# Performance work log

Measured on AMD Instinct MI355X. Metric: run time of the kernel, lower is better.

Reference implementation:

```python
import jax, jax.numpy as jnp
import numpy as np

N_NODES = 100000


def gcn_conv(x, edge_index, W, b):
    # PyG GCNConv: add self-loops, symmetric normalization D^-1/2 (A+I) D^-1/2, then linear.
    n = x.shape[0]
    loop = jnp.arange(n, dtype=edge_index.dtype)
    src = jnp.concatenate([edge_index[0], loop])
    dst = jnp.concatenate([edge_index[1], loop])
    deg = jax.ops.segment_sum(jnp.ones_like(dst, dtype=x.dtype), dst, num_segments=n)
    dinv = jnp.where(deg > 0, jax.lax.rsqrt(deg), 0.0)
    norm = dinv[src] * dinv[dst]                      # [E+N]
    h = x @ W                                          # [N, out]
    msg = h[src] * norm[:, None]                       # gather + scale
    out = jax.ops.segment_sum(msg, dst, num_segments=n)  # scatter-add
    return out + b


def forward_one(x, edge_index, W1, b1, W2, b2, fc_w, fc_b):
    x = jax.nn.relu(gcn_conv(x, edge_index, W1, b1))
    x = jax.nn.relu(gcn_conv(x, edge_index, W2, b2))
    x = jnp.mean(x, axis=0)                            # [hidden]
    return x @ fc_w.T + fc_b


def setup_inputs() -> dict:
    key = jax.random.key(0)
    ks = jax.random.split(key, 10)
    d_in, d_h = 64, 64
    E = 1600000
    s = 1.0 / np.sqrt(d_in)
    return {
        "x1": jax.random.normal(ks[0], (N_NODES, d_in), jnp.float32),
        "x2": jax.random.normal(ks[1], (N_NODES, d_in), jnp.float32),
        "edge_index1": jax.random.randint(ks[2], (2, E), 0, N_NODES, jnp.int32),
        "edge_index2": jax.random.randint(ks[3], (2, E), 0, N_NODES, jnp.int32),
        "W1": jax.random.normal(ks[4], (d_in, d_h), jnp.float32) * s,
        "b1": jnp.zeros((d_h,), jnp.float32),
        "W2": jax.random.normal(ks[5], (d_h, d_h), jnp.float32) * s,
        "b2": jnp.zeros((d_h,), jnp.float32),
        "fc_w": jax.random.normal(ks[6], (d_h, d_h), jnp.float32) * s,
        "fc_b": jnp.zeros((d_h,), jnp.float32),
    }


def reference(x1, x2, edge_index1, edge_index2, W1, b1, W2, b2, fc_w, fc_b):
    out1 = forward_one(x1, edge_index1, W1, b1, W2, b2, fc_w, fc_b)
    out2 = forward_one(x2, edge_index2, W1, b1, W2, b2, fc_w, fc_b)
    return (out1, out2)
```

## Files before the change

kernel.cpp:

```cpp
#include <hip/hip_runtime.h>


#define TPB    256
#define CHUNK  128
#define SHIFT  7
#define KMAX   1024
#define CAP    2560
#define EPB    8192
#define CPAD   16

typedef __attribute__((ext_vector_type(8))) short short8;
typedef __attribute__((ext_vector_type(4))) float f32x4;
typedef __attribute__((ext_vector_type(2))) float float2v;

struct Ctx {
    const float* X; const int* esrc; const int* edst;
    unsigned int* temp; unsigned char* Hs2; unsigned char* Hs;
    unsigned int* csr; int* row_ptr; int* degA; float* dinv; int* cursorG;
    float* P; float* P2; float* outp;
};

__device__ __forceinline__ unsigned short f2bf(float x) {
    union { float f; unsigned int i; } c; c.f = x;
    unsigned int r = c.i + 0x7FFFu + ((c.i >> 16) & 1u);
    return (unsigned short)(r >> 16);
}
__device__ __forceinline__ unsigned char f2fp8(float x) {
    int p = __builtin_amdgcn_cvt_pk_fp8_f32(x, x, 0, false);
    return (unsigned char)(p & 0xFF);
}
__device__ __forceinline__ float2v up8lo(unsigned int w) {
    return __builtin_amdgcn_cvt_pk_f32_fp8(w, false);
}
__device__ __forceinline__ float2v up8hi(unsigned int w) {
    return __builtin_amdgcn_cvt_pk_f32_fp8(w, true);
}

__global__ void k_prepW2(const float* __restrict__ W1, const float* __restrict__ W2,
                         unsigned short* __restrict__ Wt1, unsigned short* __restrict__ Wt2) {
    const float* W = blockIdx.x ? W2 : W1;
    unsigned short* Wt = blockIdx.x ? Wt2 : Wt1;
    for (int i = threadIdx.x; i < 64 * 64; i += 256) {
        int n = i >> 6, k = i & 63;
        Wt[i] = f2bf(W[k * 64 + n]);
    }
}

__global__ void k_zeroCur(Ctx c0, Ctx c1, int nb0, int K, int N) {
    int b = blockIdx.x; Ctx c = c0;
    if (b >= nb0) { c = c1; b -= nb0; }
    int i = b * blockDim.x + threadIdx.x;
    if (i < K) c.cursorG[i * CPAD] = 0;
    if (b == 0 && threadIdx.x < 64) c.Hs[(size_t)N * 64 + threadIdx.x] = 0;
}

__global__ __launch_bounds__(1024) void k_binA(Ctx c0, Ctx c1, int nb0, int E, int K) {
    __shared__ int cnt[KMAX];
    __shared__ int ofs[KMAX];
    __shared__ int segBase[KMAX];
    __shared__ unsigned int sorted[EPB];
    __shared__ unsigned short bkt[EPB];
    int b = blockIdx.x; Ctx c = c0;
    if (b >= nb0) { c = c1; b -= nb0; }
    int tid = threadIdx.x;
    cnt[tid] = 0;
    __syncthreads();
    int base = b * EPB;
    int tot = E - base; if (tot > EPB) tot = EPB;
#pragma unroll
    for (int k = 0; k < EPB / 1024; ++k) {
        int e = base + k * 1024 + tid;
        if (e < E) atomicAdd(&cnt[c.edst[e] >> SHIFT], 1);
    }
    __syncthreads();
    int v = cnt[tid];
    segBase[tid] = v;
    __syncthreads();
#pragma unroll
    for (int off = 1; off < 1024; off <<= 1) {
        int t = (tid >= off) ? segBase[tid - off] : 0;
        __syncthreads();
        segBase[tid] += t;
        __syncthreads();
    }
    ofs[tid] = segBase[tid] - v;
    __syncthreads();
    if (tid < K) {
        segBase[tid] = v ? atomicAdd(&c.cursorG[tid * CPAD], v) : 0;
    } else {
        segBase[tid] = 0;
    }
    cnt[tid] = 0;
    __syncthreads();
#pragma unroll
    for (int k = 0; k < EPB / 1024; ++k) {
        int e = base + k * 1024 + tid;
        if (e < E) {
            int d = c.edst[e];
            int bk = d >> SHIFT;
            int r = atomicAdd(&cnt[bk], 1);
            int p = ofs[bk] + r;
            sorted[p] = ((unsigned int)(d & (CHUNK - 1)) << 17) | (unsigned int)c.esrc[e];
            bkt[p] = (unsigned short)bk;
        }
    }
    __syncthreads();
    for (int p = tid; p < tot; p += 1024) {
        unsigned int vv = sorted[p];
        int bk = bkt[p];
        int pos = segBase[bk] + (p - ofs[bk]);
        if (pos < CAP) c.temp[(size_t)bk * CAP + pos] = vv;
    }
}

__global__ __launch_bounds__(256) void k_csrb(Ctx c0, Ctx c1, int nb0, int N) {
    __shared__ int deg[CHUNK];
    __shared__ int lofs[CHUNK];
    __shared__ int cur[CHUNK];
    int b = blockIdx.x; Ctx c = c0;
    if (b >= nb0) { c = c1; b -= nb0; }
    int tid = threadIdx.x;
    if (tid < CHUNK) deg[tid] = 0;
    __syncthreads();
    int cnt = c.cursorG[b * CPAD]; if (cnt > CAP) cnt = CAP;
    const size_t tb = (size_t)b * CAP;
    for (int i = tid; i < cnt; i += 256) atomicAdd(&deg[c.temp[tb + i] >> 17], 1);
    __syncthreads();
    if (tid < CHUNK) lofs[tid] = deg[tid];
    __syncthreads();
#pragma unroll
    for (int off = 1; off < CHUNK; off <<= 1) {
        int t = (tid < CHUNK && tid >= off) ? lofs[tid - off] : 0;
        __syncthreads();
        if (tid < CHUNK) lofs[tid] += t;
        __syncthreads();
    }
    int base = b * CAP;
    if (tid < CHUNK) {
        int excl = lofs[tid] - deg[tid];
        lofs[tid] = excl;
        cur[tid] = 0;
        int node = b * CHUNK + tid;
        if (node < N) {
            c.row_ptr[node] = base + excl;
            c.degA[node] = deg[tid];
            c.dinv[node] = rsqrtf((float)deg[tid] + 1.0f);
        }
    }
    __syncthreads();
    for (int i = tid; i < cnt; i += 256) {
        unsigned int p = c.temp[tb + i];
        int dl = p >> 17;
        int rank = atomicAdd(&cur[dl], 1);
        c.csr[base + lofs[dl] + rank] = (p & 0x1FFFFu) << 6;
    }
}

__device__ __forceinline__ void mfma_tail(short8 a0, short8 a1,
                                          const unsigned short* __restrict__ Wt,
                                          unsigned char* __restrict__ Hs,
                                          int row0, int r, int q, int N) {
    short8 bfrag[4][2];
#pragma unroll
    for (int ct = 0; ct < 4; ++ct)
#pragma unroll
        for (int kb = 0; kb < 2; ++kb)
            bfrag[ct][kb] = *(const short8*)(Wt + (ct * 16 + r) * 64 + q * 8 + 32 * kb);
    f32x4 acc[4];
#pragma unroll
    for (int ct = 0; ct < 4; ++ct) {
        acc[ct] = (f32x4){0.0f, 0.0f, 0.0f, 0.0f};
        acc[ct] = __builtin_amdgcn_mfma_f32_16x16x32_bf16(a0, bfrag[ct][0], acc[ct], 0, 0, 0);
        acc[ct] = __builtin_amdgcn_mfma_f32_16x16x32_bf16(a1, bfrag[ct][1], acc[ct], 0, 0, 0);
    }
#pragma unroll
    for (int reg = 0; reg < 4; ++reg) {
        int row = row0 + q * 4 + reg;
        if (row < N) {
            size_t base = (size_t)row * 64 + r;
#pragma unroll
            for (int ct = 0; ct < 4; ++ct)
                Hs[base + ct * 16] = f2fp8(acc[ct][reg]);
        }
    }
}

__global__ __launch_bounds__(256) void k_gemm1(Ctx c0, Ctx c1, int nb0,
                                               const unsigned short* __restrict__ Wt,
                                               int nTiles, int N) {
    int b = blockIdx.x; Ctx c = c0;
    if (b >= nb0) { c = c1; b -= nb0; }
    int wave = threadIdx.x >> 6, lane = threadIdx.x & 63;
    int tile = b * 4 + wave;
    if (tile >= nTiles) return;
    int r = lane & 15, q = lane >> 4;
    int row0 = tile * 16;
    int row = row0 + r;
    int rr = row < N ? row : N - 1;
    float d = c.dinv[rr];
    const float* xrow = c.X + (size_t)rr * 64 + q * 8;
    short8 a0, a1;
#pragma unroll
    for (int j = 0; j < 8; ++j) a0[j] = (short)f2bf(xrow[j] * d);
#pragma unroll
    for (int j = 0; j < 8; ++j) a1[j] = (short)f2bf(xrow[32 + j] * d);
    mfma_tail(a0, a1, Wt, c.Hs, row0, r, q, N);
}

__device__ __forceinline__ void agg_map(int bi, int nb0, int swz,
                                        const Ctx& c0, const Ctx& c1,
                                        Ctx& c, int& b) {
    if (swz) {
        int graph = (bi >> 2) & 1;
        b = ((bi >> 3) << 2) | (bi & 3);
        c = graph ? c1 : c0;
    } else {
        b = bi; c = c0;
        if (b >= nb0) { c = c1; b -= nb0; }
    }
}

__device__ __forceinline__ void agg_node2(const unsigned char* __restrict__ Hs,
                                          const unsigned int* __restrict__ csr,
                                          int beg, int deg, int maxd, int lane,
                                          unsigned int sent, float2v* acc) {
    int hbase = lane & 32;
    int hl = lane & 31;
    int g = (lane >> 4) & 1;
    unsigned int s4 = (unsigned int)((lane & 15) * 4);
    int maxs = __builtin_amdgcn_readfirstlane(maxd);
    for (int base = 0; base < maxs; base += 32) {
        unsigned int idx = (base + hl < deg) ? csr[beg + base + hl] : sent;
        int mW = maxs - base; if (mW > 32) mW = 32;
        for (int t = 0; t < mW; t += 16) {
            int lim = mW - t; if (lim > 16) lim = 16;
            unsigned int h[8];
#pragma unroll
            for (int u = 0; u < 8; ++u) {
                if (2 * u >= lim) break;
                unsigned int su = (unsigned int)__shfl((int)idx, hbase + t + 2 * u + g, 64);
                h[u] = *(const unsigned int*)(Hs + (su | s4));
            }
#pragma unroll
            for (int u = 0; u < 8; ++u) {
                if (2 * u >= lim) break;
                acc[0] += up8lo(h[u]); acc[1] += up8hi(h[u]);
            }
        }
    }
#pragma unroll
    for (int k = 0; k < 2; ++k) {
        float2v o;
        o.x = __shfl_xor(acc[k].x, 16, 64); o.y = __shfl_xor(acc[k].y, 16, 64);
        acc[k] += o;
    }
}

__global__ __launch_bounds__(256) void k_agg1(Ctx c0, Ctx c1, int nb0, int swz,
                                              const float* __restrict__ bias,
                                              const unsigned short* __restrict__ Wt2,
                                              int n) {
    __shared__ unsigned short As[8][64];
    Ctx c; int b;
    agg_map(blockIdx.x, nb0, swz, c0, c1, c, b);
    int wave = threadIdx.x >> 6, lane = threadIdx.x & 63;
    int h = lane >> 5;
    int node = b * 8 + wave * 2 + h;
    int nd = node < n ? node : 0;
    int beg = c.row_ptr[nd];
    int deg = (node < n) ? c.degA[nd] : 0;
    int od = __shfl_xor(deg, 32, 64);
    int maxd = deg > od ? deg : od;
    if (b == 0 && threadIdx.x < 64) c.Hs2[(size_t)n * 64 + threadIdx.x] = 0;
    float2v acc[2] = {{0.f, 0.f}, {0.f, 0.f}};
    agg_node2(c.Hs, c.csr, beg, deg, maxd, lane, (unsigned int)n << 6, acc);
    if (((lane >> 4) & 1) == 0) {
        int s = lane & 15;
        ushort4 o = {0, 0, 0, 0};
        if (node < n) {
            unsigned int hv = *(const unsigned int*)(c.Hs + (size_t)node * 64 + s * 4);
            float2v h0 = up8lo(hv), h1 = up8hi(hv);
            float4 bb = *(const float4*)(bias + s * 4);
            float d = c.dinv[node];
            o.x = f2bf(fmaxf(bb.x + d * (acc[0].x + h0.x), 0.0f) * d);
            o.y = f2bf(fmaxf(bb.y + d * (acc[0].y + h0.y), 0.0f) * d);
            o.z = f2bf(fmaxf(bb.z + d * (acc[1].x + h1.x), 0.0f) * d);
            o.w = f2bf(fmaxf(bb.w + d * (acc[1].y + h1.y), 0.0f) * d);
        }
        int row = wave * 2 + h;
        *(ushort4*)(&As[row][(s * 4) ^ ((row & 7) << 3)]) = o;
    }
    __syncthreads();
    {
        int r = lane & 15, q = lane >> 4;
        short8 a0 = {}, a1 = {};
        if (r < 8) {
            int sw = (r & 7) << 3;
            a0 = *(const short8*)(&As[r][(q * 8) ^ sw]);
            a1 = *(const short8*)(&As[r][(q * 8 + 32) ^ sw]);
        }
        const unsigned short* wp = Wt2 + (wave * 16 + r) * 64 + q * 8;
        short8 b0 = *(const short8*)(wp);
        short8 b1 = *(const short8*)(wp + 32);
        f32x4 acc2 = {0.0f, 0.0f, 0.0f, 0.0f};
        acc2 = __builtin_amdgcn_mfma_f32_16x16x32_bf16(a0, b0, acc2, 0, 0, 0);
        acc2 = __builtin_amdgcn_mfma_f32_16x16x32_bf16(a1, b1, acc2, 0, 0, 0);
#pragma unroll
        for (int reg = 0; reg < 4; ++reg) {
            int l = q * 4 + reg;
            int row = b * 8 + l;
            if (l < 8 && row < n)
                c.Hs2[(size_t)row * 64 + wave * 16 + r] = f2fp8(acc2[reg]);
        }
    }
}

__global__ __launch_bounds__(256) void k_agg2(Ctx c0, Ctx c1, int nb0, int swz,
                                              const float* __restrict__ bias, int n) {
    __shared__ float red[8 * 64];
    Ctx c; int b;
    agg_map(blockIdx.x, nb0, swz, c0, c1, c, b);
    int wave = threadIdx.x >> 6, lane = threadIdx.x & 63;
    int h = lane >> 5;
    int node = b * 8 + wave * 2 + h;
    int nd = node < n ? node : 0;
    int beg = c.row_ptr[nd];
    int deg = (node < n) ? c.degA[nd] : 0;
    int od = __shfl_xor(deg, 32, 64);
    int maxd = deg > od ? deg : od;
    float2v acc[2] = {{0.f, 0.f}, {0.f, 0.f}};
    agg_node2(c.Hs2, c.csr, beg, deg, maxd, lane, (unsigned int)n << 6, acc);
    if (((lane >> 4) & 1) == 0) {
        int s = lane & 15;
        float4 v = {0.f, 0.f, 0.f, 0.f};
        if (node < n) {
            unsigned int hv = *(const unsigned int*)(c.Hs2 + (size_t)node * 64 + s * 4);
            float2v h0 = up8lo(hv), h1 = up8hi(hv);
            float4 bb = *(const float4*)(bias + s * 4);
            float d = c.dinv[node];
            v.x = fmaxf(bb.x + d * (acc[0].x + h0.x), 0.0f);
            v.y = fmaxf(bb.y + d * (acc[0].y + h0.y), 0.0f);
            v.z = fmaxf(bb.z + d * (acc[1].x + h1.x), 0.0f);
            v.w = fmaxf(bb.w + d * (acc[1].y + h1.y), 0.0f);
        }
        *(float4*)(&red[(wave * 2 + h) * 64 + s * 4]) = v;
    }
    __syncthreads();
    if (threadIdx.x < 64) {
        float acc8 = 0.0f;
#pragma unroll
        for (int r = 0; r < 8; ++r) acc8 += red[r * 64 + threadIdx.x];
        c.P[(size_t)b * 64 + threadIdx.x] = acc8;
    }
}

__global__ void k_colsum(Ctx c0, Ctx c1, int nb0, int rows) {
    int b = blockIdx.x; Ctx c = c0;
    if (b >= nb0) { c = c1; b -= nb0; }
    int f = threadIdx.x;
    float acc = 0.0f;
    for (int r = b; r < rows; r += nb0) acc += c.P[(size_t)r * 64 + f];
    c.P2[b * 64 + f] = acc;
}

__global__ void k_fc(Ctx c0, Ctx c1, const float* __restrict__ fcw,
                     const float* __restrict__ fcb, int n) {
    Ctx c = blockIdx.x ? c1 : c0;
    __shared__ float S[64];
    int j = threadIdx.x;
    float s = 0.0f;
    for (int r = 0; r < 256; ++r) s += c.P2[r * 64 + j];
    S[j] = s;
    __syncthreads();
    float inv = 1.0f / (float)n;
    float acc = fcb[j];
#pragma unroll
    for (int k = 0; k < 64; ++k) acc += (S[k] * inv) * fcw[j * 64 + k];
    c.outp[j] = acc;
}

extern "C" void kernel_launch(void* const* d_in, const int* in_sizes, int n_in,
                              void* d_out, int out_size, void* d_ws, size_t ws_size,
                              hipStream_t stream) {
    const float* x[2]  = {(const float*)d_in[0], (const float*)d_in[1]};
    const int*   ei[2] = {(const int*)d_in[2], (const int*)d_in[3]};
    const float* W1  = (const float*)d_in[4];
    const float* b1  = (const float*)d_in[5];
    const float* W2  = (const float*)d_in[6];
    const float* b2  = (const float*)d_in[7];
    const float* fcw = (const float*)d_in[8];
    const float* fcb = (const float*)d_in[9];
    float* out = (float*)d_out;

    const int N  = in_sizes[0] / 64;
    const int E  = in_sizes[2] / 2;
    const int NF = N * 64;
    const int K  = (N + CHUNK - 1) / CHUNK;
    const int gGm = (N + 7) / 8;
    const int nTiles = (N + 15) / 16;
    const int gMf = (nTiles + 3) / 4;
    const int gBin = (E + EPB - 1) / EPB;
    const int gK  = (K + TPB - 1) / TPB;

    auto al = [](size_t x) { return (x + 127) & ~(size_t)127; };
    size_t tempB = (size_t)K * CAP * 4;
    size_t hs2B  = (size_t)NF + 64;
    size_t szRegion = al(tempB > hs2B ? tempB : hs2B);
    size_t szHs  = al((size_t)NF + 64);
    size_t szCsr = al((size_t)K * CAP * 4);
    size_t szRp  = al((size_t)N * 4);
    size_t szDeg = al((size_t)N * 4);
    size_t szDi  = al((size_t)N * 4);
    size_t szCu  = al((size_t)K * CPAD * 4);
    size_t szP   = al((size_t)gGm * 64 * 4);
    size_t szP2  = al((size_t)256 * 64 * 4);
    size_t setB  = szRegion + szHs + szCsr + szRp + szDeg + szDi + szCu + szP + szP2;
    size_t wtB   = 2 * al(64 * 64 * 2);
    bool batched = ws_size >= wtB + 2 * setB;

    char* base = (char*)d_ws;
    unsigned short* Wt1 = (unsigned short*)base;
    unsigned short* Wt2 = (unsigned short*)(base + al(64 * 64 * 2));

    auto mkctx = [&](int g, char* p) {
        Ctx c;
        c.X = x[g]; c.esrc = ei[g]; c.edst = ei[g] + E;
        c.temp = (unsigned int*)p; c.Hs2 = (unsigned char*)p; p += szRegion;
        c.Hs = (unsigned char*)p; p += szHs;
        c.csr = (unsigned int*)p; p += szCsr;
        c.row_ptr = (int*)p; p += szRp;
        c.degA = (int*)p; p += szDeg;
        c.dinv = (float*)p; p += szDi;
        c.cursorG = (int*)p; p += szCu;
        c.P = (float*)p; p += szP;
        c.P2 = (float*)p;
        c.outp = out + g * 64;
        return c;
    };
    char* set0 = base + wtB;
    Ctx c0 = mkctx(0, set0);
    Ctx c1 = mkctx(1, batched ? set0 + setB : set0);

    k_prepW2<<<2, 256, 0, stream>>>(W1, W2, Wt1, Wt2);

    auto pipe = [&](Ctx A, Ctx B, int mult) {
        int swz = (mult == 2 && (gGm & 3) == 0) ? 1 : 0;
        k_zeroCur<<<mult * gK, TPB, 0, stream>>>(A, B, gK, K, N);
        k_binA<<<mult * gBin, 1024, 0, stream>>>(A, B, gBin, E, K);
        k_csrb<<<mult * K, 256, 0, stream>>>(A, B, K, N);
        k_gemm1<<<mult * gMf, 256, 0, stream>>>(A, B, gMf, Wt1, nTiles, N);
        k_agg1<<<mult * gGm, 256, 0, stream>>>(A, B, gGm, swz, b1, Wt2, N);
        k_agg2<<<mult * gGm, 256, 0, stream>>>(A, B, gGm, swz, b2, N);
        k_colsum<<<mult * 256, 64, 0, stream>>>(A, B, 256, gGm);
        k_fc<<<mult, 64, 0, stream>>>(A, B, fcw, fcb, N);
    };

    if (batched) {
        pipe(c0, c1, 2);
    } else {
        pipe(c0, c0, 1);
        pipe(c1, c1, 1);
    }
}
```

Measured before the change: 304.5 us.

## Process two node pairs per wave in aggregation with interleaved gathers

```diff
diff --git a/kernel.cpp b/kernel.cpp
--- a/kernel.cpp
+++ b/kernel.cpp
@@ -220,39 +220,78 @@
     }
 }
 
-__device__ __forceinline__ void agg_node2(const unsigned char* __restrict__ Hs,
+__device__ __forceinline__ void agg_issue8(const unsigned char* __restrict__ Hs,
+                                           unsigned int idx, int slotbase, int lim,
+                                           int hbase, int g, unsigned int s4,
+                                           unsigned int* h) {
+#pragma unroll
+    for (int u = 0; u < 8; ++u) {
+        if (slotbase + 2 * u >= lim) break;
+        unsigned int su = (unsigned int)__shfl((int)idx, hbase + slotbase + 2 * u + g, 64);
+        h[u] = *(const unsigned int*)(Hs + (su | s4));
+    }
+}
+__device__ __forceinline__ void agg_cons8(const unsigned int* h, int slotbase, int lim,
+                                          float2v* acc) {
+#pragma unroll
+    for (int u = 0; u < 8; ++u) {
+        if (slotbase + 2 * u >= lim) break;
+        acc[0] += up8lo(h[u]); acc[1] += up8hi(h[u]);
+    }
+}
+
+__device__ __forceinline__ void agg_pair2(const unsigned char* __restrict__ Hs,
                                           const unsigned int* __restrict__ csr,
-                                          int beg, int deg, int maxd, int lane,
-                                          unsigned int sent, float2v* acc) {
+                                          int beg0, int deg0, int maxs0,
+                                          int beg1, int deg1, int maxs1,
+                                          int lane, unsigned int sent,
+                                          float2v* acc0, float2v* acc1) {
     int hbase = lane & 32;
     int hl = lane & 31;
     int g = (lane >> 4) & 1;
     unsigned int s4 = (unsigned int)((lane & 15) * 4);
-    int maxs = __builtin_amdgcn_readfirstlane(maxd);
-    for (int base = 0; base < maxs; base += 32) {
-        unsigned int idx = (base + hl < deg) ? csr[beg + base + hl] : sent;
-        int mW = maxs - base; if (mW > 32) mW = 32;
-        for (int t = 0; t < mW; t += 16) {
-            int lim = mW - t; if (lim > 16) lim = 16;
-            unsigned int h[8];
-#pragma unroll
-            for (int u = 0; u < 8; ++u) {
-                if (2 * u >= lim) break;
-                unsigned int su = (unsigned int)__shfl((int)idx, hbase + t + 2 * u + g, 64);
-                h[u] = *(const unsigned int*)(Hs + (su | s4));
-            }
-#pragma unroll
-            for (int u = 0; u < 8; ++u) {
-                if (2 * u >= lim) break;
-                acc[0] += up8lo(h[u]); acc[1] += up8hi(h[u]);
-            }
+    unsigned int idx0 = (hl < deg0) ? csr[beg0 + hl] : sent;
+    unsigned int idx1 = (hl < deg1) ? csr[beg1 + hl] : sent;
+    int lim0 = maxs0 > 32 ? 32 : maxs0;
+    int lim1 = maxs1 > 32 ? 32 : maxs1;
+    unsigned int h0[8], h1[8];
+    agg_issue8(Hs, idx0, 0, lim0, hbase, g, s4, h0);
+    agg_issue8(Hs, idx1, 0, lim1, hbase, g, s4, h1);
+    agg_cons8(h0, 0, lim0, acc0);
+    if (lim0 > 16) agg_issue8(Hs, idx0, 16, lim0, hbase, g, s4, h0);
+    agg_cons8(h1, 0, lim1, acc1);
+    if (lim1 > 16) agg_issue8(Hs, idx1, 16, lim1, hbase, g, s4, h1);
+    if (lim0 > 16) agg_cons8(h0, 16, lim0, acc0);
+    if (lim1 > 16) agg_cons8(h1, 16, lim1, acc1);
+    for (int base = 32; base < maxs0; base += 32) {
+        unsigned int idx = (base + hl < deg0) ? csr[beg0 + base + hl] : sent;
+        int lim = maxs0 - base; if (lim > 32) lim = 32;
+        unsigned int hh[8];
+        agg_issue8(Hs, idx, 0, lim, hbase, g, s4, hh);
+        agg_cons8(hh, 0, lim, acc0);
+        if (lim > 16) {
+            agg_issue8(Hs, idx, 16, lim, hbase, g, s4, hh);
+            agg_cons8(hh, 16, lim, acc0);
+        }
+    }
+    for (int base = 32; base < maxs1; base += 32) {
+        unsigned int idx = (base + hl < deg1) ? csr[beg1 + base + hl] : sent;
+        int lim = maxs1 - base; if (lim > 32) lim = 32;
+        unsigned int hh[8];
+        agg_issue8(Hs, idx, 0, lim, hbase, g, s4, hh);
+        agg_cons8(hh, 0, lim, acc1);
+        if (lim > 16) {
+            agg_issue8(Hs, idx, 16, lim, hbase, g, s4, hh);
+            agg_cons8(hh, 16, lim, acc1);
         }
     }
 #pragma unroll
     for (int k = 0; k < 2; ++k) {
         float2v o;
-        o.x = __shfl_xor(acc[k].x, 16, 64); o.y = __shfl_xor(acc[k].y, 16, 64);
-        acc[k] += o;
+        o.x = __shfl_xor(acc0[k].x, 16, 64); o.y = __shfl_xor(acc0[k].y, 16, 64);
+        acc0[k] += o;
+        o.x = __shfl_xor(acc1[k].x, 16, 64); o.y = __shfl_xor(acc1[k].y, 16, 64);
+        acc1[k] += o;
     }
 }
 
@@ -260,45 +299,56 @@
                                               const float* __restrict__ bias,
                                               const unsigned short* __restrict__ Wt2,
                                               int n) {
-    __shared__ unsigned short As[8][64];
+    __shared__ unsigned short As[16][64];
     Ctx c; int b;
     agg_map(blockIdx.x, nb0, swz, c0, c1, c, b);
     int wave = threadIdx.x >> 6, lane = threadIdx.x & 63;
     int h = lane >> 5;
-    int node = b * 8 + wave * 2 + h;
-    int nd = node < n ? node : 0;
-    int beg = c.row_ptr[nd];
-    int deg = (node < n) ? c.degA[nd] : 0;
-    int od = __shfl_xor(deg, 32, 64);
-    int maxd = deg > od ? deg : od;
+    int nbase = b * 16 + wave * 4;
+    int node0 = nbase + h;
+    int node1 = nbase + 2 + h;
+    int nd0 = node0 < n ? node0 : 0;
+    int nd1 = node1 < n ? node1 : 0;
+    int beg0 = c.row_ptr[nd0];
+    int beg1 = c.row_ptr[nd1];
+    int deg0 = (node0 < n) ? c.degA[nd0] : 0;
+    int deg1 = (node1 < n) ? c.degA[nd1] : 0;
+    int od0 = __shfl_xor(deg0, 32, 64); int m0 = deg0 > od0 ? deg0 : od0;
+    int od1 = __shfl_xor(deg1, 32, 64); int m1 = deg1 > od1 ? deg1 : od1;
+    int maxs0 = __builtin_amdgcn_readfirstlane(m0);
+    int maxs1 = __builtin_amdgcn_readfirstlane(m1);
     if (b == 0 && threadIdx.x < 64) c.Hs2[(size_t)n * 64 + threadIdx.x] = 0;
-    float2v acc[2] = {{0.f, 0.f}, {0.f, 0.f}};
-    agg_node2(c.Hs, c.csr, beg, deg, maxd, lane, (unsigned int)n << 6, acc);
+    float2v acc0[2] = {{0.f, 0.f}, {0.f, 0.f}};
+    float2v acc1[2] = {{0.f, 0.f}, {0.f, 0.f}};
+    agg_pair2(c.Hs, c.csr, beg0, deg0, maxs0, beg1, deg1, maxs1,
+              lane, (unsigned int)n << 6, acc0, acc1);
     if (((lane >> 4) & 1) == 0) {
         int s = lane & 15;
-        ushort4 o = {0, 0, 0, 0};
-        if (node < n) {
-            unsigned int hv = *(const unsigned int*)(c.Hs + (size_t)node * 64 + s * 4);
-            float2v h0 = up8lo(hv), h1 = up8hi(hv);
-            float4 bb = *(const float4*)(bias + s * 4);
-            float d = c.dinv[node];
-            o.x = f2bf(fmaxf(bb.x + d * (acc[0].x + h0.x), 0.0f) * d);
-            o.y = f2bf(fmaxf(bb.y + d * (acc[0].y + h0.y), 0.0f) * d);
-            o.z = f2bf(fmaxf(bb.z + d * (acc[1].x + h1.x), 0.0f) * d);
-            o.w = f2bf(fmaxf(bb.w + d * (acc[1].y + h1.y), 0.0f) * d);
-        }
-        int row = wave * 2 + h;
-        *(ushort4*)(&As[row][(s * 4) ^ ((row & 7) << 3)]) = o;
+#pragma unroll
+        for (int pr = 0; pr < 2; ++pr) {
+            const float2v* ac = pr ? acc1 : acc0;
+            int node = nbase + pr * 2 + h;
+            ushort4 o = {0, 0, 0, 0};
+            if (node < n) {
+                unsigned int hv = *(const unsigned int*)(c.Hs + (size_t)node * 64 + s * 4);
+                float2v h0 = up8lo(hv), h1 = up8hi(hv);
+                float4 bb = *(const float4*)(bias + s * 4);
+                float d = c.dinv[node];
+                o.x = f2bf(fmaxf(bb.x + d * (ac[0].x + h0.x), 0.0f) * d);
+                o.y = f2bf(fmaxf(bb.y + d * (ac[0].y + h0.y), 0.0f) * d);
+                o.z = f2bf(fmaxf(bb.z + d * (ac[1].x + h1.x), 0.0f) * d);
+                o.w = f2bf(fmaxf(bb.w + d * (ac[1].y + h1.y), 0.0f) * d);
+            }
+            int row = wave * 4 + pr * 2 + h;
+            *(ushort4*)(&As[row][(s * 4) ^ ((row & 7) << 3)]) = o;
+        }
     }
     __syncthreads();
     {
         int r = lane & 15, q = lane >> 4;
-        short8 a0 = {}, a1 = {};
-        if (r < 8) {
-            int sw = (r & 7) << 3;
-            a0 = *(const short8*)(&As[r][(q * 8) ^ sw]);
-            a1 = *(const short8*)(&As[r][(q * 8 + 32) ^ sw]);
-        }
+        int sw = (r & 7) << 3;
+        short8 a0 = *(const short8*)(&As[r][(q * 8) ^ sw]);
+        short8 a1 = *(const short8*)(&As[r][(q * 8 + 32) ^ sw]);
         const unsigned short* wp = Wt2 + (wave * 16 + r) * 64 + q * 8;
         short8 b0 = *(const short8*)(wp);
         short8 b1 = *(const short8*)(wp + 32);
@@ -308,8 +358,8 @@
 #pragma unroll
         for (int reg = 0; reg < 4; ++reg) {
             int l = q * 4 + reg;
-            int row = b * 8 + l;
-            if (l < 8 && row < n)
+            int row = b * 16 + l;
+            if (row < n)
                 c.Hs2[(size_t)row * 64 + wave * 16 + r] = f2fp8(acc2[reg]);
         }
     }
@@ -317,40 +367,54 @@
 
 __global__ __launch_bounds__(256) void k_agg2(Ctx c0, Ctx c1, int nb0, int swz,
                                               const float* __restrict__ bias, int n) {
-    __shared__ float red[8 * 64];
+    __shared__ float red[16 * 64];
     Ctx c; int b;
     agg_map(blockIdx.x, nb0, swz, c0, c1, c, b);
     int wave = threadIdx.x >> 6, lane = threadIdx.x & 63;
     int h = lane >> 5;
-    int node = b * 8 + wave * 2 + h;
-    int nd = node < n ? node : 0;
-    int beg = c.row_ptr[nd];
-    int deg = (node < n) ? c.degA[nd] : 0;
-    int od = __shfl_xor(deg, 32, 64);
-    int maxd = deg > od ? deg : od;
-    float2v acc[2] = {{0.f, 0.f}, {0.f, 0.f}};
-    agg_node2(c.Hs2, c.csr, beg, deg, maxd, lane, (unsigned int)n << 6, acc);
+    int nbase = b * 16 + wave * 4;
+    int node0 = nbase + h;
+    int node1 = nbase + 2 + h;
+    int nd0 = node0 < n ? node0 : 0;
+    int nd1 = node1 < n ? node1 : 0;
+    int beg0 = c.row_ptr[nd0];
+    int beg1 = c.row_ptr[nd1];
+    int deg0 = (node0 < n) ? c.degA[nd0] : 0;
+    int deg1 = (node1 < n) ? c.degA[nd1] : 0;
+    int od0 = __shfl_xor(deg0, 32, 64); int m0 = deg0 > od0 ? deg0 : od0;
+    int od1 = __shfl_xor(deg1, 32, 64); int m1 = deg1 > od1 ? deg1 : od1;
+    int maxs0 = __builtin_amdgcn_readfirstlane(m0);
+    int maxs1 = __builtin_amdgcn_readfirstlane(m1);
+    float2v acc0[2] = {{0.f, 0.f}, {0.f, 0.f}};
+    float2v acc1[2] = {{0.f, 0.f}, {0.f, 0.f}};
+    agg_pair2(c.Hs2, c.csr, beg0, deg0, maxs0, beg1, deg1, maxs1,
+              lane, (unsigned int)n << 6, acc0, acc1);
     if (((lane >> 4) & 1) == 0) {
         int s = lane & 15;
-        float4 v = {0.f, 0.f, 0.f, 0.f};
-        if (node < n) {
-            unsigned int hv = *(const unsigned int*)(c.Hs2 + (size_t)node * 64 + s * 4);
-            float2v h0 = up8lo(hv), h1 = up8hi(hv);
-            float4 bb = *(const float4*)(bias + s * 4);
-            float d = c.dinv[node];
-            v.x = fmaxf(bb.x + d * (acc[0].x + h0.x), 0.0f);
-            v.y = fmaxf(bb.y + d * (acc[0].y + h0.y), 0.0f);
-            v.z = fmaxf(bb.z + d * (acc[1].x + h1.x), 0.0f);
-            v.w = fmaxf(bb.w + d * (acc[1].y + h1.y), 0.0f);
-        }
-        *(float4*)(&red[(wave * 2 + h) * 64 + s * 4]) = v;
+#pragma unroll
+        for (int pr = 0; pr < 2; ++pr) {
+            const float2v* ac = pr ? acc1 : acc0;
+            int node = nbase + pr * 2 + h;
+            float4 v = {0.f, 0.f, 0.f, 0.f};
+            if (node < n) {
+                unsigned int hv = *(const unsigned int*)(c.Hs2 + (size_t)node * 64 + s * 4);
+                float2v h0 = up8lo(hv), h1 = up8hi(hv);
+                float4 bb = *(const float4*)(bias + s * 4);
+                float d = c.dinv[node];
+                v.x = fmaxf(bb.x + d * (ac[0].x + h0.x), 0.0f);
+                v.y = fmaxf(bb.y + d * (ac[0].y + h0.y), 0.0f);
+                v.z = fmaxf(bb.z + d * (ac[1].x + h1.x), 0.0f);
+                v.w = fmaxf(bb.w + d * (ac[1].y + h1.y), 0.0f);
+            }
+            *(float4*)(&red[(wave * 4 + pr * 2 + h) * 64 + s * 4]) = v;
+        }
     }
     __syncthreads();
     if (threadIdx.x < 64) {
-        float acc8 = 0.0f;
-#pragma unroll
-        for (int r = 0; r < 8; ++r) acc8 += red[r * 64 + threadIdx.x];
-        c.P[(size_t)b * 64 + threadIdx.x] = acc8;
+        float acc16 = 0.0f;
+#pragma unroll
+        for (int r = 0; r < 16; ++r) acc16 += red[r * 64 + threadIdx.x];
+        c.P[(size_t)b * 64 + threadIdx.x] = acc16;
     }
 }
 
@@ -396,7 +460,8 @@
     const int E  = in_sizes[2] / 2;
     const int NF = N * 64;
     const int K  = (N + CHUNK - 1) / CHUNK;
-    const int gGm = (N + 7) / 8;
+    const int gGm  = (N + 15) / 16;
+    const int gGmP = (gGm + 3) & ~3;
     const int nTiles = (N + 15) / 16;
     const int gMf = (nTiles + 3) / 4;
     const int gBin = (E + EPB - 1) / EPB;
@@ -412,7 +477,7 @@
     size_t szDeg = al((size_t)N * 4);
     size_t szDi  = al((size_t)N * 4);
     size_t szCu  = al((size_t)K * CPAD * 4);
-    size_t szP   = al((size_t)gGm * 64 * 4);
+    size_t szP   = al((size_t)gGmP * 64 * 4);
     size_t szP2  = al((size_t)256 * 64 * 4);
     size_t setB  = szRegion + szHs + szCsr + szRp + szDeg + szDi + szCu + szP + szP2;
     size_t wtB   = 2 * al(64 * 64 * 2);
@@ -444,14 +509,14 @@
     k_prepW2<<<2, 256, 0, stream>>>(W1, W2, Wt1, Wt2);
 
     auto pipe = [&](Ctx A, Ctx B, int mult) {
-        int swz = (mult == 2 && (gGm & 3) == 0) ? 1 : 0;
+        int swz = (mult == 2) ? 1 : 0;
         k_zeroCur<<<mult * gK, TPB, 0, stream>>>(A, B, gK, K, N);
         k_binA<<<mult * gBin, 1024, 0, stream>>>(A, B, gBin, E, K);
         k_csrb<<<mult * K, 256, 0, stream>>>(A, B, K, N);
         k_gemm1<<<mult * gMf, 256, 0, stream>>>(A, B, gMf, Wt1, nTiles, N);
-        k_agg1<<<mult * gGm, 256, 0, stream>>>(A, B, gGm, swz, b1, Wt2, N);
-        k_agg2<<<mult * gGm, 256, 0, stream>>>(A, B, gGm, swz, b2, N);
-        k_colsum<<<mult * 256, 64, 0, stream>>>(A, B, 256, gGm);
+        k_agg1<<<mult * gGmP, 256, 0, stream>>>(A, B, gGmP, swz, b1, Wt2, N);
+        k_agg2<<<mult * gGmP, 256, 0, stream>>>(A, B, gGmP, swz, b2, N);
+        k_colsum<<<mult * 256, 64, 0, stream>>>(A, B, 256, gGmP);
         k_fc<<<mult, 64, 0, stream>>>(A, B, fcw, fcb, N);
     };
 
```

Measured after the change: 285.4 us. -6.3%, faster.
